# Optimization experiments

Measured on AMD Instinct MI355X. Metric: run time of the kernel, lower is better.

Reference implementation:

```python
import jax, jax.numpy as jnp
import numpy as np

EPS = 1e-5


def _bn(x, g, b):
    # training-mode BatchNorm2d: batch statistics over (N,H,W), biased variance
    m = x.mean(axis=(0, 2, 3), keepdims=True)
    v = x.var(axis=(0, 2, 3), keepdims=True)
    return g[None, :, None, None] * (x - m) * jax.lax.rsqrt(v + EPS) + b[None, :, None, None]


def _pw(x, w):
    # 1x1 conv, no bias: w [O, C]
    return jnp.einsum('oc,bchw->bohw', w, x)


def setup_inputs() -> dict:
    key = jax.random.key(0)
    ks = jax.random.split(key, 23)
    B, C, H, W = 8, 128, 112, 112
    O, Hd = 256, 512
    r, qd = C // 4, C // 8

    def n(k, shape, s=0.05):
        return jax.random.normal(k, shape, jnp.float32) * s

    return dict(
        x=jax.random.normal(ks[0], (B, C, H, W), jnp.float32),
        dw_w=n(ks[1], (C, 1, 3, 3), 0.2),
        bn1_g=1.0 + n(ks[2], (C,)), bn1_b=n(ks[3], (C,)),
        se_w1=n(ks[4], (r, C), 0.1), se_b1=n(ks[5], (r,)),
        se_w2=n(ks[6], (C, r), 0.1), se_b2=n(ks[7], (C,)),
        q_w=n(ks[8], (qd, C), 0.1), q_b=n(ks[9], (qd,)),
        k_w=n(ks[10], (qd, C), 0.1), k_b=n(ks[11], (qd,)),
        v_w=n(ks[12], (C, C), 0.1), v_b=n(ks[13], (C,)),
        pw_w=n(ks[14], (O, C), 0.1),
        bn2_g=1.0 + n(ks[15], (O,)), bn2_b=n(ks[16], (O,)),
        m1_w=n(ks[17], (Hd, O), 0.1),
        bn3_g=1.0 + n(ks[18], (Hd,)), bn3_b=n(ks[19], (Hd,)),
        m2_w=n(ks[20], (O, Hd), 0.1),
        bn4_g=1.0 + n(ks[21], (O,)), bn4_b=n(ks[22], (O,)),
    )


def reference(x, dw_w, bn1_g, bn1_b, se_w1, se_b1, se_w2, se_b2,
              q_w, q_b, k_w, k_b, v_w, v_b, pw_w, bn2_g, bn2_b,
              m1_w, bn3_g, bn3_b, m2_w, bn4_g, bn4_b):
    C = x.shape[1]
    # token mixer: depthwise stride-2 conv + BN
    h = jax.lax.conv_general_dilated(
        x, dw_w, window_strides=(2, 2), padding=((1, 1), (1, 1)),
        feature_group_count=C, dimension_numbers=('NCHW', 'OIHW', 'NCHW'))
    h = _bn(h, bn1_g, bn1_b)
    # squeeze-excite
    s = h.mean(axis=(2, 3))                        # [B, C]
    s = jax.nn.relu(s @ se_w1.T + se_b1)
    s = jax.nn.sigmoid(s @ se_w2.T + se_b2)
    h = h * s[:, :, None, None]
    # global attention (full NxN, no scaling, residual add)
    B, _, Hh, Ww = h.shape
    N = Hh * Ww
    hf = h.reshape(B, C, N)                        # [B, C, N]
    q = jnp.einsum('dc,bcn->bnd', q_w, hf) + q_b   # [B, N, C/8]
    k = jnp.einsum('dc,bcn->bdn', k_w, hf) + k_b[None, :, None]  # [B, C/8, N]
    attn = jax.nn.softmax(jnp.einsum('bnd,bdm->bnm', q, k), axis=-1)  # [B, N, N]
    v = jnp.einsum('oc,bcn->bon', v_w, hf) + v_b[None, :, None]       # [B, C, N]
    h = jnp.einsum('bcn,bmn->bcm', v, attn).reshape(B, C, Hh, Ww) + h
    # 1x1 projection + BN
    h = _bn(_pw(h, pw_w), bn2_g, bn2_b)            # [B, O, Hh, Ww]
    # channel mixer: 1x1 -> BN -> GELU -> 1x1 -> BN (no residual per source)
    m = jax.nn.gelu(_bn(_pw(h, m1_w), bn3_g, bn3_b), approximate=False)
    out = _bn(_pw(m, m2_w), bn4_g, bn4_b)
    return out
```

## Files before the change

kernel.cpp:

```cpp
#include <hip/hip_runtime.h>
#include <math.h>

namespace {

constexpr int kB = 8;
constexpr int kC = 128;
constexpr int kHin = 112, kWin = 112;
constexpr int kHout = 56, kWout = 56;
constexpr int kN = kHout * kWout;
constexpr int kO = 256;
constexpr int kHd = 512;
constexpr int kR = 32;
constexpr float kEps = 1e-5f;

typedef __attribute__((ext_vector_type(8))) short short8v;
typedef __attribute__((ext_vector_type(4))) float f32x4;
typedef __attribute__((ext_vector_type(16))) float f32x16;
typedef __attribute__((ext_vector_type(4))) uint uint4v;

__device__ __forceinline__ ushort f2bf(float f) {
  uint u = __float_as_uint(f);
  uint r = (u + 0x7FFFu + ((u >> 16) & 1u)) >> 16;
  return (ushort)r;
}
__device__ __forceinline__ uint pack2bf(float a, float b) {
  return (uint)f2bf(a) | ((uint)f2bf(b) << 16);
}
__device__ __forceinline__ float bf2f(ushort u) {
  return __uint_as_float((uint)u << 16);
}
__device__ __forceinline__ float gelu_fast(float x) {
  float y = 0.7978845608f * (x + 0.044715f * x * x * x);
  float e = __expf(2.0f * y);
  float t = 1.0f - 2.0f / (e + 1.0f);
  return 0.5f * x * (1.0f + t);
}

__global__ __launch_bounds__(256) void dwconv_kernel(
    const float* __restrict__ x, const float* __restrict__ w,
    float* __restrict__ h0, float* __restrict__ sums, float* __restrict__ ssqs) {
  int bc = blockIdx.x;
  int c = bc % kC;
  const float* xp = x + (size_t)bc * (kHin * kWin);
  __shared__ float xs[kHin * kWin];
  for (int i = threadIdx.x * 4; i < kHin * kWin; i += 1024) {
    *(float4*)&xs[i] = *(const float4*)&xp[i];
  }
  float wr[9];
#pragma unroll
  for (int i = 0; i < 9; ++i) wr[i] = w[c * 9 + i];
  __syncthreads();
  float lsum = 0.f, lssq = 0.f;
  for (int i = threadIdx.x; i < kN; i += 256) {
    int oy = i / kWout, ox = i - oy * kWout;
    int iy0 = 2 * oy - 1, ix0 = 2 * ox - 1;
    float acc = 0.f;
#pragma unroll
    for (int ky = 0; ky < 3; ++ky) {
      int iy = iy0 + ky;
      if (iy < 0 || iy >= kHin) continue;
#pragma unroll
      for (int kx = 0; kx < 3; ++kx) {
        int ix = ix0 + kx;
        if (ix < 0 || ix >= kWin) continue;
        acc += xs[iy * kWin + ix] * wr[ky * 3 + kx];
      }
    }
    h0[(size_t)bc * kN + i] = acc;
    lsum += acc;
    lssq += acc * acc;
  }
  __shared__ float rs[256], rq[256];
  rs[threadIdx.x] = lsum; rq[threadIdx.x] = lssq;
  __syncthreads();
  for (int s = 128; s > 0; s >>= 1) {
    if (threadIdx.x < s) { rs[threadIdx.x] += rs[threadIdx.x + s]; rq[threadIdx.x] += rq[threadIdx.x + s]; }
    __syncthreads();
  }
  if (threadIdx.x == 0) { sums[bc] = rs[0]; ssqs[bc] = rq[0]; }
}

__global__ __launch_bounds__(128) void se_kernel(
    const float* __restrict__ sums, const float* __restrict__ ssqs,
    const float* __restrict__ bn1_g, const float* __restrict__ bn1_b,
    const float* __restrict__ se_w1, const float* __restrict__ se_b1,
    const float* __restrict__ se_w2, const float* __restrict__ se_b2,
    float* __restrict__ scale_bc, float* __restrict__ bias_bc) {
  int b = blockIdx.x, c = threadIdx.x;
  __shared__ float sin_[kC], s1[kR], alf[kC], bet[kC];
  float ts = 0.f, tq = 0.f;
  for (int bb = 0; bb < kB; ++bb) { ts += sums[bb * kC + c]; tq += ssqs[bb * kC + c]; }
  float inv = 1.0f / ((float)kB * (float)kN);
  float mean = ts * inv;
  float var = tq * inv - mean * mean;
  float a = bn1_g[c] * rsqrtf(var + kEps);
  float be = bn1_b[c] - mean * a;
  alf[c] = a; bet[c] = be;
  sin_[c] = a * (sums[b * kC + c] * (1.0f / kN)) + be;
  __syncthreads();
  if (c < kR) {
    float acc = se_b1[c];
    for (int j = 0; j < kC; ++j) acc += se_w1[c * kC + j] * sin_[j];
    s1[c] = fmaxf(acc, 0.f);
  }
  __syncthreads();
  float acc = se_b2[c];
  for (int j = 0; j < kR; ++j) acc += se_w2[c * kR + j] * s1[j];
  float sg = 1.0f / (1.0f + expf(-acc));
  scale_bc[b * kC + c] = alf[c] * sg;
  bias_bc[b * kC + c] = bet[c] * sg;
}

__global__ __launch_bounds__(256) void scale_tm_kernel(
    const float* __restrict__ h0, const float* __restrict__ sc,
    const float* __restrict__ bi, ushort* __restrict__ hfT16) {
  __shared__ float T[32][33];
  int b = blockIdx.z;
  int c0 = blockIdx.y * 32;
  int n0 = blockIdx.x * 32;
  int tid = threadIdx.x;
  int r = tid >> 3, seg = tid & 7;
  int c = c0 + r;
  int bc = b * kC + c;
  float s = sc[bc], t = bi[bc];
  size_t idx = (size_t)bc * kN + n0 + seg * 4;
  float4 v = *(const float4*)&h0[idx];
  v.x = s * v.x + t; v.y = s * v.y + t; v.z = s * v.z + t; v.w = s * v.w + t;
  T[seg * 4 + 0][r] = v.x; T[seg * 4 + 1][r] = v.y;
  T[seg * 4 + 2][r] = v.z; T[seg * 4 + 3][r] = v.w;
  __syncthreads();
  float4 o = make_float4(T[r][seg * 4], T[r][seg * 4 + 1], T[r][seg * 4 + 2], T[r][seg * 4 + 3]);
  uint2 ou = make_uint2(pack2bf(o.x, o.y), pack2bf(o.z, o.w));
  *(uint2*)&hfT16[((size_t)b * kN + n0 + r) * kC + c0 + seg * 4] = ou;
}

__global__ void wconv_kernel(const float* __restrict__ vw, const float* __restrict__ pww,
                             const float* __restrict__ m2w,
                             ushort* __restrict__ ov, ushort* __restrict__ opw,
                             ushort* __restrict__ om2) {
  int stride = gridDim.x * 256;
  int i0 = blockIdx.x * 256 + threadIdx.x;
  for (int i = i0; i < 128 * 128; i += stride) ov[i] = f2bf(vw[i]);
  for (int i = i0; i < 256 * 128; i += stride) opw[i] = f2bf(pww[i]);
  for (int i = i0; i < 256 * 512; i += stride) om2[i] = f2bf(m2w[i]);
}

__global__ __launch_bounds__(256) void foldm1_kernel(
    const float* __restrict__ m1w, const float* __restrict__ a2,
    const float* __restrict__ b2, ushort* __restrict__ wf, float* __restrict__ bias1) {
  int r = blockIdx.x;
  int c = threadIdx.x;
  float w = m1w[r * 256 + c];
  wf[r * 256 + c] = f2bf(w * a2[c]);
  __shared__ float red[256];
  red[c] = w * b2[c];
  __syncthreads();
  for (int s = 128; s > 0; s >>= 1) {
    if (c < s) red[c] += red[c + s];
    __syncthreads();
  }
  if (c == 0) bias1[r] = red[0];
}

__global__ __launch_bounds__(256) void qk_kernel(
    const ushort* __restrict__ hfT16, const float* __restrict__ q_w,
    const float* __restrict__ q_b, const float* __restrict__ k_w,
    const float* __restrict__ k_b, ushort* __restrict__ qA, ushort* __restrict__ kA) {
  __shared__ float Wl[32][128];
  __shared__ float Xl[64][129];
  int b = blockIdx.y;
  int n0 = blockIdx.x * 64;
  int tid = threadIdx.x;
  for (int u = tid; u < 1024; u += 256) {
    int r = u >> 5, seg = u & 31;
    const float* src = (r < 16) ? &q_w[r * 128 + seg * 4] : &k_w[(r - 16) * 128 + seg * 4];
    float4 v = *(const float4*)src;
    *(float4*)&Wl[r][seg * 4] = v;
  }
  const ushort* Xb = hfT16 + ((size_t)b * kN + n0) * kC;
  for (int u = tid; u < 1024; u += 256) {
    int r = u >> 4, seg = u & 15;
    short8v v = *(const short8v*)&Xb[(size_t)r * kC + seg * 8];
#pragma unroll
    for (int j = 0; j < 8; ++j) Xl[r][seg * 8 + j] = bf2f((ushort)v[j]);
  }
  __syncthreads();
  int tt = tid & 63, og = tid >> 6;
  float acc[8] = {};
  for (int k = 0; k < 128; ++k) {
    float xx = Xl[tt][k];
#pragma unroll
    for (int j = 0; j < 8; ++j) acc[j] += xx * Wl[og * 8 + j][k];
  }
  float scl = (og < 2) ? 1.0f : 1.44269504f;
  uint pk[4];
#pragma unroll
  for (int j2 = 0; j2 < 4; ++j2) {
    int m = og * 8 + j2 * 2;
    float b0 = (m < 16) ? q_b[m] : k_b[m - 16];
    float b1 = (m + 1 < 16) ? q_b[m + 1] : k_b[m + 1 - 16];
    pk[j2] = pack2bf((acc[j2 * 2] + b0) * scl, (acc[j2 * 2 + 1] + b1) * scl);
  }
  int n = n0 + tt;
  int t = n >> 5, r = n & 31, h = og & 1;
  ushort* dst = (og < 2 ? qA : kA) + (size_t)b * kN * 16 + (((size_t)t * 2 + h) * 32 + r) * 8;
  *(uint4*)dst = make_uint4(pk[0], pk[1], pk[2], pk[3]);
}

template <int M, int K, int INMODE, int OUTMODE, int STATS>
__global__ __launch_bounds__(256) void mfma_gemm_kernel(
    const ushort* __restrict__ Wb, const float* __restrict__ Xf,
    const ushort* __restrict__ Xh, ushort* __restrict__ Yh,
    const float* __restrict__ bias, float* __restrict__ psumO,
    float* __restrict__ pssqO) {
  constexpr int BM = 128, BN = 128, BK = 64, LDW = 72;
  __shared__ alignas(16) ushort Wl[BM * LDW];
  __shared__ alignas(16) ushort Xl[BN * LDW];
  int b = blockIdx.z;
  int n0 = blockIdx.x * BN;
  int m0 = blockIdx.y * BM;
  int tid = threadIdx.x;
  int w = tid >> 6, lane = tid & 63;
  int wm = w >> 1, wn = w & 1;
  int lg = lane >> 4, lq = lane & 15;
  f32x4 acc[4][4];
#pragma unroll
  for (int i = 0; i < 4; ++i)
#pragma unroll
    for (int j = 0; j < 4; ++j) acc[i][j] = (f32x4){0.f, 0.f, 0.f, 0.f};

  int wseg = tid & 7;
  int xseg = tid & 15;

  for (int kk = 0; kk < K; kk += BK) {
    __syncthreads();
#pragma unroll
    for (int u = 0; u < 4; ++u) {
      int row = (tid + u * 256) >> 3;
      short8v wv = *(const short8v*)&Wb[(size_t)(m0 + row) * K + kk + wseg * 8];
      *(short8v*)&Wl[row * LDW + wseg * 8] = wv;
    }
    if (INMODE == 0) {
      const float* Xb = Xf + (size_t)b * kN * K;
#pragma unroll
      for (int u = 0; u < 8; ++u) {
        int row = (tid + u * 256) >> 4;
        int n = n0 + row;
        float4 xv = make_float4(0.f, 0.f, 0.f, 0.f);
        if (n < kN) xv = *(const float4*)&Xb[(size_t)n * K + kk + xseg * 4];
        *(uint2*)&Xl[row * LDW + xseg * 4] =
            make_uint2(pack2bf(xv.x, xv.y), pack2bf(xv.z, xv.w));
      }
    } else {
      const ushort* Xb = Xh + (size_t)b * kN * K;
#pragma unroll
      for (int u = 0; u < 4; ++u) {
        int idx = tid + u * 256;
        int row = idx >> 3, seg = idx & 7;
        int n = n0 + row;
        short8v xv = (short8v){0, 0, 0, 0, 0, 0, 0, 0};
        if (n < kN) xv = *(const short8v*)&Xb[(size_t)n * K + kk + seg * 8];
        *(short8v*)&Xl[row * LDW + seg * 8] = xv;
      }
    }
    __syncthreads();
#pragma unroll
    for (int kh = 0; kh < BK; kh += 32) {
      short8v af[4], bfr[4];
#pragma unroll
      for (int f = 0; f < 4; ++f) {
        af[f] = *(const short8v*)&Wl[(wm * 64 + f * 16 + lq) * LDW + kh + 8 * lg];
        bfr[f] = *(const short8v*)&Xl[(wn * 64 + f * 16 + lq) * LDW + kh + 8 * lg];
      }
#pragma unroll
      for (int fi = 0; fi < 4; ++fi)
#pragma unroll
        for (int fj = 0; fj < 4; ++fj)
          acc[fi][fj] = __builtin_amdgcn_mfma_f32_16x16x32_bf16(af[fi], bfr[fj], acc[fi][fj], 0, 0, 0);
    }
  }
  if (OUTMODE == 1) {
    ushort* Yb = Yh + (size_t)b * M * kN;
#pragma unroll
    for (int fi = 0; fi < 4; ++fi) {
#pragma unroll
      for (int r = 0; r < 4; ++r) {
        int m = m0 + wm * 64 + fi * 16 + 4 * lg + r;
        float bv = bias ? bias[m] : 0.f;
#pragma unroll
        for (int fj = 0; fj < 4; ++fj) {
          int n = n0 + wn * 64 + fj * 16 + lq;
          if (n < kN) {
            int t = n >> 5, nl = n & 31;
            int pp = (nl & ~12) | ((nl & 4) << 1) | ((nl & 8) >> 1);
            Yb[(((size_t)t * 4 + (pp >> 3)) * 128 + m) * 8 + (pp & 7)] =
                f2bf(acc[fi][fj][r] + bv);
          }
        }
      }
    }
  } else {
    float tsum[16], tssq[16];
    if (STATS) {
#pragma unroll
      for (int i = 0; i < 16; ++i) { tsum[i] = 0.f; tssq[i] = 0.f; }
    }
    ushort* Yb = Yh + (size_t)b * kN * M;
#pragma unroll
    for (int fj = 0; fj < 4; ++fj) {
      int n = n0 + wn * 64 + fj * 16 + lq;
      if (n < kN) {
#pragma unroll
        for (int fi = 0; fi < 4; ++fi) {
          int mb = m0 + wm * 64 + fi * 16 + 4 * lg;
          f32x4 v = acc[fi][fj];
          if (bias) {
            v[0] += bias[mb]; v[1] += bias[mb + 1];
            v[2] += bias[mb + 2]; v[3] += bias[mb + 3];
          }
          if (STATS) {
#pragma unroll
            for (int r = 0; r < 4; ++r) {
              float val = v[r];
              tsum[fi * 4 + r] += val;
              tssq[fi * 4 + r] += val * val;
            }
          }
          *(uint2*)&Yb[(size_t)n * M + mb] =
              make_uint2(pack2bf(v[0], v[1]), pack2bf(v[2], v[3]));
        }
      }
    }
    if (STATS) {
      __syncthreads();
      float* Ssum = (float*)Wl;
      float* Sssq = (float*)Xl;
      int col = wn * 16 + lq;
#pragma unroll
      for (int fi = 0; fi < 4; ++fi)
#pragma unroll
        for (int r = 0; r < 4; ++r) {
          int ml = wm * 64 + fi * 16 + 4 * lg + r;
          Ssum[ml * 33 + col] = tsum[fi * 4 + r];
          Sssq[ml * 33 + col] = tssq[fi * 4 + r];
        }
      __syncthreads();
      int ml = tid & 127;
      const float* src = (tid < 128) ? Ssum : Sssq;
      float a = 0.f;
#pragma unroll
      for (int j = 0; j < 32; ++j) a += src[ml * 33 + j];
      int bidx = blockIdx.x * gridDim.z + blockIdx.z;
      if (tid < 128) psumO[(size_t)bidx * M + m0 + ml] = a;
      else           pssqO[(size_t)bidx * M + m0 + ml] = a;
    }
  }
}

__global__ __launch_bounds__(256) void attn_mfma32_kernel(
    const ushort* __restrict__ qA, const ushort* __restrict__ kA,
    const ushort* __restrict__ vA, const ushort* __restrict__ hfT16,
    ushort* __restrict__ attT) {
  int b = blockIdx.x;
  int n0 = blockIdx.y * 32;
  int tid = threadIdx.x;
  int w = tid >> 6;
  int lane = tid & 63;
  int l31 = lane & 31;
  int hi = lane >> 5;

  __shared__ float lbuf[4][32], lfin[32];
  __shared__ float obuf[32][132];

  const ushort* qAb = qA + (size_t)b * kN * 16;
  const ushort* kAb = kA + (size_t)b * kN * 16;
  const ushort* vAb = vA + (size_t)b * kN * 128;

  short8v qf = *(const short8v*)&qAb[(((size_t)blockIdx.y * 2 + hi) * 32 + l31) * 8];

  f32x16 z16 = {0.f,0.f,0.f,0.f,0.f,0.f,0.f,0.f,0.f,0.f,0.f,0.f,0.f,0.f,0.f,0.f};
  f32x16 acc[4];
#pragma unroll
  for (int cg = 0; cg < 4; ++cg) acc[cg] = z16;
  f32x16 accl = z16;
  const short kOneBf = (short)0x3F80;
  short8v ones = {kOneBf, kOneBf, kOneBf, kOneBf, kOneBf, kOneBf, kOneBf, kOneBf};

  short8v kf_cur = *(const short8v*)&kAb[(((size_t)w * 2 + hi) * 32 + l31) * 8];

  for (int t = w; t < 98; t += 4) {
    const ushort* vt = vAb + (size_t)t * 4 * 128 * 8;
    short8v va[4], vb2[4];
#pragma unroll
    for (int cg = 0; cg < 4; ++cg) {
      va[cg]  = *(const short8v*)&vt[((size_t)hi * 128 + cg * 32 + l31) * 8];
      vb2[cg] = *(const short8v*)&vt[(((size_t)(2 + hi)) * 128 + cg * 32 + l31) * 8];
    }
    int tn = t + 4;
    short8v kf_nxt = kf_cur;
    if (tn < 98)
      kf_nxt = *(const short8v*)&kAb[(((size_t)tn * 2 + hi) * 32 + l31) * 8];

    f32x16 s = __builtin_amdgcn_mfma_f32_32x32x16_bf16(kf_cur, qf, z16, 0, 0, 0);

    uint wd[8];
#pragma unroll
    for (int i = 0; i < 8; ++i) {
      float pl = exp2f(s[2 * i]);
      float ph = exp2f(s[2 * i + 1]);
      asm("v_cvt_pk_bf16_f32 %0, %1, %2" : "=v"(wd[i]) : "v"(pl), "v"(ph));
    }

    uint4v u1 = {wd[0], wd[1], wd[2], wd[3]};
    uint4v u2 = {wd[4], wd[5], wd[6], wd[7]};
    short8v P1 = __builtin_bit_cast(short8v, u1);
    short8v P2 = __builtin_bit_cast(short8v, u2);
    accl = __builtin_amdgcn_mfma_f32_32x32x16_bf16(ones, P1, accl, 0, 0, 0);
    accl = __builtin_amdgcn_mfma_f32_32x32x16_bf16(ones, P2, accl, 0, 0, 0);
#pragma unroll
    for (int cg = 0; cg < 4; ++cg) {
      acc[cg] = __builtin_amdgcn_mfma_f32_32x32x16_bf16(va[cg], P1, acc[cg], 0, 0, 0);
      acc[cg] = __builtin_amdgcn_mfma_f32_32x32x16_bf16(vb2[cg], P2, acc[cg], 0, 0, 0);
    }
    kf_cur = kf_nxt;
  }

  if (lane < 32) lbuf[w][lane] = accl[0];
  __syncthreads();
  if (w == 0 && lane < 32) {
    float L = 0.f;
#pragma unroll
    for (int j = 0; j < 4; ++j) L += lbuf[j][lane];
    lfin[lane] = L;
  }

  for (int turn = 0; turn < 4; ++turn) {
    if (w == turn) {
#pragma unroll
      for (int cg = 0; cg < 4; ++cg)
#pragma unroll
        for (int rr = 0; rr < 4; ++rr) {
          int c = cg * 32 + 8 * rr + 4 * hi;
          float4 vv;
          vv.x = acc[cg][4 * rr + 0];
          vv.y = acc[cg][4 * rr + 1];
          vv.z = acc[cg][4 * rr + 2];
          vv.w = acc[cg][4 * rr + 3];
          if (turn == 0) {
            *(float4*)&obuf[l31][c] = vv;
          } else {
            float4 o = *(const float4*)&obuf[l31][c];
            o.x += vv.x; o.y += vv.y; o.z += vv.z; o.w += vv.w;
            *(float4*)&obuf[l31][c] = o;
          }
        }
    }
    __syncthreads();
  }

  int q = tid >> 3;
  int cs = (tid & 7) * 16;
  float linv = 1.0f / lfin[q];
  size_t nidx = (size_t)b * kN + n0 + q;
  const ushort* hrow = &hfT16[nidx * kC + cs];
  ushort* arow = &attT[nidx * kC + cs];
#pragma unroll
  for (int cc = 0; cc < 16; cc += 4) {
    uint2 hu = *(const uint2*)&hrow[cc];
    float r0 = __uint_as_float(hu.x << 16);
    float r1 = __uint_as_float(hu.x & 0xFFFF0000u);
    float r2 = __uint_as_float(hu.y << 16);
    float r3 = __uint_as_float(hu.y & 0xFFFF0000u);
    float o0 = obuf[q][cs + cc + 0] * linv + r0;
    float o1 = obuf[q][cs + cc + 1] * linv + r1;
    float o2 = obuf[q][cs + cc + 2] * linv + r2;
    float o3 = obuf[q][cs + cc + 3] * linv + r3;
    *(uint2*)&arow[cc] = make_uint2(pack2bf(o0, o1), pack2bf(o2, o3));
  }
}

template <int CH, int NP>
__global__ __launch_bounds__(256) void bnfin_kernel(
    const float* __restrict__ psum, const float* __restrict__ pssq,
    const float* __restrict__ g, const float* __restrict__ bt,
    float* __restrict__ alpha, float* __restrict__ beta) {
  int cl = threadIdx.x & 63;
  int pg = threadIdx.x >> 6;
  int ch = blockIdx.x * 64 + cl;
  float s = 0.f, q = 0.f;
#pragma unroll 10
  for (int p = pg; p < NP; p += 4) {
    s += psum[(size_t)p * CH + ch];
    q += pssq[(size_t)p * CH + ch];
  }
  __shared__ float Ss[4][64], Sq[4][64];
  Ss[pg][cl] = s; Sq[pg][cl] = q;
  __syncthreads();
  if (pg == 0) {
    s = Ss[0][cl] + Ss[1][cl] + Ss[2][cl] + Ss[3][cl];
    q = Sq[0][cl] + Sq[1][cl] + Sq[2][cl] + Sq[3][cl];
    float inv = 1.0f / ((float)kB * (float)kN);
    float mean = s * inv;
    float var = q * inv - mean * mean;
    float a = g[ch] * rsqrtf(var + kEps);
    alpha[ch] = a;
    beta[ch] = bt[ch] - mean * a;
  }
}

__global__ __launch_bounds__(256) void gelupass_kernel(
    const ushort* __restrict__ m1o, const float* __restrict__ a3,
    const float* __restrict__ b3, ushort* __restrict__ g) {
  size_t total8 = (size_t)kB * kN * kHd / 8;
  for (size_t i = (size_t)blockIdx.x * 256 + threadIdx.x; i < total8;
       i += (size_t)gridDim.x * 256) {
    int c8 = (int)(i & 63) * 8;
    short8v x = ((const short8v*)m1o)[i];
    float4 a0 = *(const float4*)&a3[c8];
    float4 a1 = *(const float4*)&a3[c8 + 4];
    float4 b0 = *(const float4*)&b3[c8];
    float4 b1 = *(const float4*)&b3[c8 + 4];
    float y0 = gelu_fast(a0.x * bf2f((ushort)x[0]) + b0.x);
    float y1 = gelu_fast(a0.y * bf2f((ushort)x[1]) + b0.y);
    float y2 = gelu_fast(a0.z * bf2f((ushort)x[2]) + b0.z);
    float y3 = gelu_fast(a0.w * bf2f((ushort)x[3]) + b0.w);
    float y4 = gelu_fast(a1.x * bf2f((ushort)x[4]) + b1.x);
    float y5 = gelu_fast(a1.y * bf2f((ushort)x[5]) + b1.y);
    float y6 = gelu_fast(a1.z * bf2f((ushort)x[6]) + b1.z);
    float y7 = gelu_fast(a1.w * bf2f((ushort)x[7]) + b1.w);
    uint4v o = {pack2bf(y0, y1), pack2bf(y2, y3), pack2bf(y4, y5), pack2bf(y6, y7)};
    ((uint4v*)g)[i] = o;
  }
}

__global__ __launch_bounds__(256) void bnout_t_kernel(
    const ushort* __restrict__ X, const float* __restrict__ alpha,
    const float* __restrict__ beta, float* __restrict__ out) {
  __shared__ float T[32][33];
  int b = blockIdx.z;
  int c0 = blockIdx.y * 32;
  int n0 = blockIdx.x * 32;
  int tid = threadIdx.x;
  int r = tid >> 3, seg = tid & 7;
  uint2 u = *(const uint2*)&X[((size_t)b * kN + n0 + r) * kO + c0 + seg * 4];
  float x0 = __uint_as_float(u.x << 16);
  float x1 = __uint_as_float(u.x & 0xFFFF0000u);
  float x2 = __uint_as_float(u.y << 16);
  float x3 = __uint_as_float(u.y & 0xFFFF0000u);
  float4 a = *(const float4*)&alpha[c0 + seg * 4];
  float4 bb = *(const float4*)&beta[c0 + seg * 4];
  T[seg * 4 + 0][r] = a.x * x0 + bb.x;
  T[seg * 4 + 1][r] = a.y * x1 + bb.y;
  T[seg * 4 + 2][r] = a.z * x2 + bb.z;
  T[seg * 4 + 3][r] = a.w * x3 + bb.w;
  __syncthreads();
  float4 o = make_float4(T[r][seg * 4], T[r][seg * 4 + 1], T[r][seg * 4 + 2], T[r][seg * 4 + 3]);
  *(float4*)&out[((size_t)b * kO + c0 + r) * kN + n0 + seg * 4] = o;
}

}

extern "C" void kernel_launch(void* const* d_in, const int* in_sizes, int n_in,
                              void* d_out, int out_size, void* d_ws, size_t ws_size,
                              hipStream_t stream) {
  const float* x     = (const float*)d_in[0];
  const float* dw_w  = (const float*)d_in[1];
  const float* bn1_g = (const float*)d_in[2];
  const float* bn1_b = (const float*)d_in[3];
  const float* se_w1 = (const float*)d_in[4];
  const float* se_b1 = (const float*)d_in[5];
  const float* se_w2 = (const float*)d_in[6];
  const float* se_b2 = (const float*)d_in[7];
  const float* q_w   = (const float*)d_in[8];
  const float* q_b   = (const float*)d_in[9];
  const float* k_w   = (const float*)d_in[10];
  const float* k_b   = (const float*)d_in[11];
  const float* v_w   = (const float*)d_in[12];
  const float* v_b   = (const float*)d_in[13];
  const float* pw_w  = (const float*)d_in[14];
  const float* bn2_g = (const float*)d_in[15];
  const float* bn2_b = (const float*)d_in[16];
  const float* m1_w  = (const float*)d_in[17];
  const float* bn3_g = (const float*)d_in[18];
  const float* bn3_b = (const float*)d_in[19];
  const float* m2_w  = (const float*)d_in[20];
  const float* bn4_g = (const float*)d_in[21];
  const float* bn4_b = (const float*)d_in[22];
  float* out = (float*)d_out;
  float* ws = (float*)d_ws;

  const size_t BCN = (size_t)kB * kC * kN;
  const size_t E8 = BCN / 8;

  float* h0      = ws;
  ushort* hfT16  = (ushort*)(ws + BCN);
  ushort* vA16   = (ushort*)(ws + 2 * BCN);
  ushort* qA16   = (ushort*)(ws + 2 * BCN + BCN / 2);
  ushort* kA16   = qA16 + (size_t)kB * kN * 16;
  ushort* attT16 = (ushort*)(ws + 2 * BCN + 5 * (BCN / 8));
  ushort* p16    = (ushort*)(ws + 3 * BCN + E8);
  ushort* m1o16  = (ushort*)(ws + 4 * BCN + E8);
  ushort* g16    = (ushort*)ws;
  ushort* m2o16  = (ushort*)(ws + 2 * BCN);
  float* wbase = ws + 6 * BCN + E8;
  ushort* wv16  = (ushort*)wbase;
  ushort* wpw16 = wv16 + 128 * 128;
  ushort* wm216 = wpw16 + 256 * 128;
  ushort* wm1f  = wm216 + 256 * 512;
  float* psum  = wbase + 155648;
  float* pssq  = psum + 131072;
  float* bias1 = pssq + 131072;
  float* smal  = bias1 + 512;
  float* sums  = smal;
  float* ssqs  = smal + 1024;
  float* sc_bc = smal + 2048;
  float* bi_bc = smal + 3072;
  float* a2 = smal + 4096; float* b2 = a2 + kO;
  float* a3 = b2 + kO;     float* b3 = a3 + kHd;
  float* a4 = b3 + kHd;    float* b4 = a4 + kO;

  wconv_kernel<<<512, 256, 0, stream>>>(v_w, pw_w, m2_w, wv16, wpw16, wm216);
  dwconv_kernel<<<kB * kC, 256, 0, stream>>>(x, dw_w, h0, sums, ssqs);
  se_kernel<<<kB, 128, 0, stream>>>(sums, ssqs, bn1_g, bn1_b, se_w1, se_b1, se_w2, se_b2,
                                    sc_bc, bi_bc);
  scale_tm_kernel<<<dim3(98, 4, kB), 256, 0, stream>>>(h0, sc_bc, bi_bc, hfT16);
  qk_kernel<<<dim3(49, kB), 256, 0, stream>>>(hfT16, q_w, q_b, k_w, k_b, qA16, kA16);
  mfma_gemm_kernel<128, 128, 1, 1, 0><<<dim3(25, 1, kB), 256, 0, stream>>>(
      wv16, nullptr, hfT16, vA16, v_b, nullptr, nullptr);
  attn_mfma32_kernel<<<dim3(kB, kN / 32), 256, 0, stream>>>(qA16, kA16, vA16, hfT16, attT16);
  mfma_gemm_kernel<256, 128, 1, 2, 1><<<dim3(25, 2, kB), 256, 0, stream>>>(
      wpw16, nullptr, attT16, p16, nullptr, psum, pssq);
  bnfin_kernel<256, 200><<<4, 256, 0, stream>>>(psum, pssq, bn2_g, bn2_b, a2, b2);
  foldm1_kernel<<<512, 256, 0, stream>>>(m1_w, a2, b2, wm1f, bias1);
  mfma_gemm_kernel<512, 256, 1, 2, 1><<<dim3(25, 4, kB), 256, 0, stream>>>(
      wm1f, nullptr, p16, m1o16, bias1, psum, pssq);
  bnfin_kernel<512, 200><<<8, 256, 0, stream>>>(psum, pssq, bn3_g, bn3_b, a3, b3);
  gelupass_kernel<<<2048, 256, 0, stream>>>(m1o16, a3, b3, g16);
  mfma_gemm_kernel<256, 512, 1, 2, 1><<<dim3(25, 2, kB), 256, 0, stream>>>(
      wm216, nullptr, g16, m2o16, nullptr, psum, pssq);
  bnfin_kernel<256, 200><<<4, 256, 0, stream>>>(psum, pssq, bn4_g, bn4_b, a4, b4);
  bnout_t_kernel<<<dim3(98, 8, kB), 256, 0, stream>>>(m2o16, a4, b4, out);
}
```

Measured before the change: 215.9 us.

## Store depthwise conv output as bf16 and remap GEMM blocks for XCD locality

```diff
diff --git a/kernel.cpp b/kernel.cpp
--- a/kernel.cpp
+++ b/kernel.cpp
@@ -38,7 +38,7 @@
 
 __global__ __launch_bounds__(256) void dwconv_kernel(
     const float* __restrict__ x, const float* __restrict__ w,
-    float* __restrict__ h0, float* __restrict__ sums, float* __restrict__ ssqs) {
+    ushort* __restrict__ h0b, float* __restrict__ sums, float* __restrict__ ssqs) {
   int bc = blockIdx.x;
   int c = bc % kC;
   const float* xp = x + (size_t)bc * (kHin * kWin);
@@ -66,7 +66,7 @@
         acc += xs[iy * kWin + ix] * wr[ky * 3 + kx];
       }
     }
-    h0[(size_t)bc * kN + i] = acc;
+    h0b[(size_t)bc * kN + i] = f2bf(acc);
     lsum += acc;
     lssq += acc * acc;
   }
@@ -112,7 +112,7 @@
 }
 
 __global__ __launch_bounds__(256) void scale_tm_kernel(
-    const float* __restrict__ h0, const float* __restrict__ sc,
+    const ushort* __restrict__ h0b, const float* __restrict__ sc,
     const float* __restrict__ bi, ushort* __restrict__ hfT16) {
   __shared__ float T[32][33];
   int b = blockIdx.z;
@@ -124,10 +124,15 @@
   int bc = b * kC + c;
   float s = sc[bc], t = bi[bc];
   size_t idx = (size_t)bc * kN + n0 + seg * 4;
-  float4 v = *(const float4*)&h0[idx];
-  v.x = s * v.x + t; v.y = s * v.y + t; v.z = s * v.z + t; v.w = s * v.w + t;
-  T[seg * 4 + 0][r] = v.x; T[seg * 4 + 1][r] = v.y;
-  T[seg * 4 + 2][r] = v.z; T[seg * 4 + 3][r] = v.w;
+  uint2 hv = *(const uint2*)&h0b[idx];
+  float v0 = __uint_as_float(hv.x << 16);
+  float v1 = __uint_as_float(hv.x & 0xFFFF0000u);
+  float v2 = __uint_as_float(hv.y << 16);
+  float v3 = __uint_as_float(hv.y & 0xFFFF0000u);
+  T[seg * 4 + 0][r] = s * v0 + t;
+  T[seg * 4 + 1][r] = s * v1 + t;
+  T[seg * 4 + 2][r] = s * v2 + t;
+  T[seg * 4 + 3][r] = s * v3 + t;
   __syncthreads();
   float4 o = make_float4(T[r][seg * 4], T[r][seg * 4 + 1], T[r][seg * 4 + 2], T[r][seg * 4 + 3]);
   uint2 ou = make_uint2(pack2bf(o.x, o.y), pack2bf(o.z, o.w));
@@ -207,7 +212,7 @@
   *(uint4*)dst = make_uint4(pk[0], pk[1], pk[2], pk[3]);
 }
 
-template <int M, int K, int INMODE, int OUTMODE, int STATS>
+template <int M, int K, int INMODE, int OUTMODE, int STATS, int YT>
 __global__ __launch_bounds__(256) void mfma_gemm_kernel(
     const ushort* __restrict__ Wb, const float* __restrict__ Xf,
     const ushort* __restrict__ Xh, ushort* __restrict__ Yh,
@@ -216,9 +221,15 @@
   constexpr int BM = 128, BN = 128, BK = 64, LDW = 72;
   __shared__ alignas(16) ushort Wl[BM * LDW];
   __shared__ alignas(16) ushort Xl[BN * LDW];
-  int b = blockIdx.z;
-  int n0 = blockIdx.x * BN;
-  int m0 = blockIdx.y * BM;
+  int bid = blockIdx.x;
+  int xcd = bid & 7;
+  int s = bid >> 3;
+  int y = s % YT;
+  int pairg = xcd * 25 + s / YT;
+  int nt = pairg % 25;
+  int b = pairg / 25;
+  int n0 = nt * BN;
+  int m0 = y * BM;
   int tid = threadIdx.x;
   int w = tid >> 6, lane = tid & 63;
   int wm = w >> 1, wn = w & 1;
@@ -350,9 +361,8 @@
       float a = 0.f;
 #pragma unroll
       for (int j = 0; j < 32; ++j) a += src[ml * 33 + j];
-      int bidx = blockIdx.x * gridDim.z + blockIdx.z;
-      if (tid < 128) psumO[(size_t)bidx * M + m0 + ml] = a;
-      else           pssqO[(size_t)bidx * M + m0 + ml] = a;
+      if (tid < 128) psumO[(size_t)pairg * M + m0 + ml] = a;
+      else           pssqO[(size_t)pairg * M + m0 + ml] = a;
     }
   }
 }
@@ -592,7 +602,7 @@
   const size_t BCN = (size_t)kB * kC * kN;
   const size_t E8 = BCN / 8;
 
-  float* h0      = ws;
+  ushort* h0b    = (ushort*)ws;
   ushort* hfT16  = (ushort*)(ws + BCN);
   ushort* vA16   = (ushort*)(ws + 2 * BCN);
   ushort* qA16   = (ushort*)(ws + 2 * BCN + BCN / 2);
@@ -620,23 +630,23 @@
   float* a4 = b3 + kHd;    float* b4 = a4 + kO;
 
   wconv_kernel<<<512, 256, 0, stream>>>(v_w, pw_w, m2_w, wv16, wpw16, wm216);
-  dwconv_kernel<<<kB * kC, 256, 0, stream>>>(x, dw_w, h0, sums, ssqs);
+  dwconv_kernel<<<kB * kC, 256, 0, stream>>>(x, dw_w, h0b, sums, ssqs);
   se_kernel<<<kB, 128, 0, stream>>>(sums, ssqs, bn1_g, bn1_b, se_w1, se_b1, se_w2, se_b2,
                                     sc_bc, bi_bc);
-  scale_tm_kernel<<<dim3(98, 4, kB), 256, 0, stream>>>(h0, sc_bc, bi_bc, hfT16);
+  scale_tm_kernel<<<dim3(98, 4, kB), 256, 0, stream>>>(h0b, sc_bc, bi_bc, hfT16);
   qk_kernel<<<dim3(49, kB), 256, 0, stream>>>(hfT16, q_w, q_b, k_w, k_b, qA16, kA16);
-  mfma_gemm_kernel<128, 128, 1, 1, 0><<<dim3(25, 1, kB), 256, 0, stream>>>(
+  mfma_gemm_kernel<128, 128, 1, 1, 0, 1><<<200, 256, 0, stream>>>(
       wv16, nullptr, hfT16, vA16, v_b, nullptr, nullptr);
   attn_mfma32_kernel<<<dim3(kB, kN / 32), 256, 0, stream>>>(qA16, kA16, vA16, hfT16, attT16);
-  mfma_gemm_kernel<256, 128, 1, 2, 1><<<dim3(25, 2, kB), 256, 0, stream>>>(
+  mfma_gemm_kernel<256, 128, 1, 2, 1, 2><<<400, 256, 0, stream>>>(
       wpw16, nullptr, attT16, p16, nullptr, psum, pssq);
   bnfin_kernel<256, 200><<<4, 256, 0, stream>>>(psum, pssq, bn2_g, bn2_b, a2, b2);
   foldm1_kernel<<<512, 256, 0, stream>>>(m1_w, a2, b2, wm1f, bias1);
-  mfma_gemm_kernel<512, 256, 1, 2, 1><<<dim3(25, 4, kB), 256, 0, stream>>>(
+  mfma_gemm_kernel<512, 256, 1, 2, 1, 4><<<800, 256, 0, stream>>>(
       wm1f, nullptr, p16, m1o16, bias1, psum, pssq);
   bnfin_kernel<512, 200><<<8, 256, 0, stream>>>(psum, pssq, bn3_g, bn3_b, a3, b3);
   gelupass_kernel<<<2048, 256, 0, stream>>>(m1o16, a3, b3, g16);
-  mfma_gemm_kernel<256, 512, 1, 2, 1><<<dim3(25, 2, kB), 256, 0, stream>>>(
+  mfma_gemm_kernel<256, 512, 1, 2, 1, 2><<<400, 256, 0, stream>>>(
       wm216, nullptr, g16, m2o16, nullptr, psum, pssq);
   bnfin_kernel<256, 200><<<4, 256, 0, stream>>>(psum, pssq, bn4_g, bn4_b, a4, b4);
   bnout_t_kernel<<<dim3(98, 8, kB), 256, 0, stream>>>(m2o16, a4, b4, out);
```

New measurement: 213.8 us. No clear change (-1.0%).
